# Optimization experiments

Hardware: AMD Instinct MI355X
Metric: run time of the kernel (lower is better)

Reference implementation:

```python
import jax, jax.numpy as jnp
import numpy as np

B, L_HIST, N_VARS, L_FUT = 32, 96, 862, 96
D_MODEL, D_INNER, D_STATE, D_CONV, DT_RANK, D_FF, E_LAYERS = 512, 512, 32, 2, 32, 512, 2
EPS = 1e-5


def _ln(x, w, b):
    m = x.mean(-1, keepdims=True)
    v = ((x - m) ** 2).mean(-1, keepdims=True)
    return (x - m) * jax.lax.rsqrt(v + EPS) * w + b


def _mamba(x, in_w, conv_w, conv_b, x_w, dt_w, dt_b, A_log, D, out_w):
    # x: [B, T, d_model]; standard mamba-ssm selective-scan block (inference)
    Bb, T, _ = x.shape
    u, z = jnp.split(x @ in_w, 2, axis=-1)                      # [B,T,E] each
    uc = jnp.transpose(u, (0, 2, 1))                            # [B,E,T]
    uc = jax.lax.conv_general_dilated(
        uc, conv_w[:, None, :], (1,), [(D_CONV - 1, 0)],
        dimension_numbers=('NCH', 'OIH', 'NCH'),
        feature_group_count=D_INNER)                            # causal depthwise conv
    u = jax.nn.silu(jnp.transpose(uc, (0, 2, 1)) + conv_b)      # [B,T,E]
    dt, Bm, Cm = jnp.split(u @ x_w, [DT_RANK, DT_RANK + D_STATE], axis=-1)
    delta = jax.nn.softplus(dt @ dt_w + dt_b)                   # [B,T,E]
    A = -jnp.exp(A_log)                                         # [E,S]

    def step(h, inp):
        d_t, u_t, B_t, C_t = inp                                # [B,E],[B,E],[B,S],[B,S]
        h = jnp.exp(d_t[..., None] * A) * h + (d_t * u_t)[..., None] * B_t[:, None, :]
        return h, jnp.einsum('bes,bs->be', h, C_t)

    h0 = jnp.zeros((Bb, D_INNER, D_STATE), x.dtype)
    _, ys = jax.lax.scan(step, h0, (delta.transpose(1, 0, 2), u.transpose(1, 0, 2),
                                    Bm.transpose(1, 0, 2), Cm.transpose(1, 0, 2)))
    y = ys.transpose(1, 0, 2) + u * D
    return (y * jax.nn.silu(z)) @ out_w


def _forward(history_data, emb_w, emb_b, m_in_w, m_conv_w, m_conv_b, m_x_w,
             m_dt_w, m_dt_b, m_A_log, m_D, m_out_w, ffn_w1, ffn_b1, ffn_w2,
             ffn_b2, norm1_w, norm1_b, norm2_w, norm2_b, normf_w, normf_b,
             proj_w, proj_b):
    x_enc = history_data[..., 0]                                # [B,L,N]
    means = jax.lax.stop_gradient(x_enc.mean(1, keepdims=True))
    x_enc = x_enc - means
    stdev = jnp.sqrt(x_enc.var(axis=1, keepdims=True) + EPS)
    x_enc = x_enc / stdev
    x = jnp.transpose(x_enc, (0, 2, 1)) @ emb_w + emb_b         # [B,N,d_model] (inverted embed)
    for l in range(E_LAYERS):
        fwd = _mamba(x, m_in_w[l, 0], m_conv_w[l, 0], m_conv_b[l, 0], m_x_w[l, 0],
                     m_dt_w[l, 0], m_dt_b[l, 0], m_A_log[l, 0], m_D[l, 0], m_out_w[l, 0])
        rev = _mamba(x[:, ::-1], m_in_w[l, 1], m_conv_w[l, 1], m_conv_b[l, 1], m_x_w[l, 1],
                     m_dt_w[l, 1], m_dt_b[l, 1], m_A_log[l, 1], m_D[l, 1], m_out_w[l, 1])[:, ::-1]
        x = _ln(x + fwd + rev, norm1_w[l], norm1_b[l])
        y = jax.nn.relu(x @ ffn_w1[l] + ffn_b1[l]) @ ffn_w2[l] + ffn_b2[l]
        x = _ln(x + y, norm2_w[l], norm2_b[l])
    x = _ln(x, normf_w, normf_b)
    dec = jnp.transpose(x @ proj_w + proj_b, (0, 2, 1))         # [B,L_FUT,N]
    dec = dec * stdev[:, 0][:, None, :] + means[:, 0][:, None, :]
    return dec[..., None]                                       # [B,L_FUT,N,1]


def setup_inputs() -> dict:
    key = jax.random.key(0)
    ks = jax.random.split(key, 16)
    def rn(k, shape, s=0.02):
        return jax.random.normal(k, shape, jnp.float32) * s
    M = (E_LAYERS, 2)
    inp = {}
    inp['history_data'] = jax.random.normal(ks[0], (B, L_HIST, N_VARS, 1), jnp.float32)
    inp['emb_w'] = rn(ks[1], (L_HIST, D_MODEL))
    inp['emb_b'] = jnp.zeros((D_MODEL,), jnp.float32)
    inp['m_in_w'] = rn(ks[2], M + (D_MODEL, 2 * D_INNER))
    inp['m_conv_w'] = rn(ks[3], M + (D_INNER, D_CONV), 0.1)
    inp['m_conv_b'] = jnp.zeros(M + (D_INNER,), jnp.float32)
    inp['m_x_w'] = rn(ks[4], M + (D_INNER, DT_RANK + 2 * D_STATE))
    inp['m_dt_w'] = rn(ks[5], M + (DT_RANK, D_INNER), 0.1)
    inp['m_dt_b'] = jnp.full(M + (D_INNER,), -4.0, jnp.float32)
    a = jnp.log(jnp.arange(1, D_STATE + 1, dtype=jnp.float32))
    inp['m_A_log'] = jnp.broadcast_to(a, M + (D_INNER, D_STATE))
    inp['m_D'] = jnp.ones(M + (D_INNER,), jnp.float32)
    inp['m_out_w'] = rn(ks[6], M + (D_INNER, D_MODEL))
    inp['ffn_w1'] = rn(ks[7], (E_LAYERS, D_MODEL, D_FF))
    inp['ffn_b1'] = jnp.zeros((E_LAYERS, D_FF), jnp.float32)
    inp['ffn_w2'] = rn(ks[8], (E_LAYERS, D_FF, D_MODEL))
    inp['ffn_b2'] = jnp.zeros((E_LAYERS, D_MODEL), jnp.float32)
    inp['norm1_w'] = jnp.ones((E_LAYERS, D_MODEL), jnp.float32)
    inp['norm1_b'] = jnp.zeros((E_LAYERS, D_MODEL), jnp.float32)
    inp['norm2_w'] = jnp.ones((E_LAYERS, D_MODEL), jnp.float32)
    inp['norm2_b'] = jnp.zeros((E_LAYERS, D_MODEL), jnp.float32)
    inp['normf_w'] = jnp.ones((D_MODEL,), jnp.float32)
    inp['normf_b'] = jnp.zeros((D_MODEL,), jnp.float32)
    inp['proj_w'] = rn(ks[9], (D_MODEL, L_FUT))
    inp['proj_b'] = jnp.zeros((L_FUT,), jnp.float32)
    return inp


def reference(history_data, emb_w, emb_b, m_in_w, m_conv_w, m_conv_b, m_x_w,
              m_dt_w, m_dt_b, m_A_log, m_D, m_out_w, ffn_w1, ffn_b1, ffn_w2,
              ffn_b2, norm1_w, norm1_b, norm2_w, norm2_b, normf_w, normf_b,
              proj_w, proj_b):
    return _forward(history_data, emb_w, emb_b, m_in_w, m_conv_w, m_conv_b, m_x_w,
                    m_dt_w, m_dt_b, m_A_log, m_D, m_out_w, ffn_w1, ffn_b1, ffn_w2,
                    ffn_b2, norm1_w, norm1_b, norm2_w, norm2_b, normf_w, normf_b,
                    proj_w, proj_b)
```

## Files before the change

kernel.cpp:

```cpp
#include <hip/hip_runtime.h>
#include <math.h>

#define BATCH 32
#define LHIST 96
#define NVARS 862
#define LFUT  96
#define DMODEL 512
#define DINNER 512
#define DSTATE 32
#define DTRANK 32
#define SCAN_C 16
#define SCAN_TC ((NVARS + SCAN_C - 1) / SCAN_C)

typedef short short8 __attribute__((ext_vector_type(8)));
typedef float floatx4 __attribute__((ext_vector_type(4)));
typedef unsigned short ushort;

#define LOG2E 1.44269504088896f

static __device__ __forceinline__ ushort f2b(float f) {
    unsigned u = __builtin_bit_cast(unsigned, f);
    unsigned r = (u + 0x7FFFu + ((u >> 16) & 1u)) >> 16;
    return (ushort)r;
}
static __device__ __forceinline__ float b2f(ushort h) {
    unsigned u = ((unsigned)h) << 16;
    return __builtin_bit_cast(float, u);
}

__global__ void meanstd_k(const float* __restrict__ hist, ushort* __restrict__ xinb,
                          float* __restrict__ meanb, float* __restrict__ stdb,
                          int b0, int CB) {
    int idx = blockIdx.x * blockDim.x + threadIdx.x;
    if (idx >= CB * NVARS) return;
    int b = b0 + idx / NVARS, n = idx % NVARS;
    const float* p = hist + (size_t)b * LHIST * NVARS + n;
    float s = 0.f;
    for (int l = 0; l < LHIST; l++) s += p[(size_t)l * NVARS];
    float mean = s * (1.f / LHIST);
    float v = 0.f;
    for (int l = 0; l < LHIST; l++) { float d = p[(size_t)l * NVARS] - mean; v += d * d; }
    v *= (1.f / LHIST);
    float sd = sqrtf(v + 1e-5f);
    float inv = 1.f / sd;
    meanb[idx] = mean;
    stdb[idx]  = sd;
    ushort* o = xinb + (size_t)idx * LHIST;
    for (int l = 0; l < LHIST; l++) o[l] = f2b((p[(size_t)l * NVARS] - mean) * inv);
}

__global__ void castT_k(const float* __restrict__ W, ushort* __restrict__ Wt,
                        int K, int N, int P) {
    size_t idx = (size_t)blockIdx.x * blockDim.x + threadIdx.x;
    if (idx >= (size_t)P * K * N) return;
    size_t kn = (size_t)K * N;
    int p = (int)(idx / kn);
    int rem = (int)(idx % kn);
    int k = rem / N, n = rem % N;
    Wt[(size_t)p * kn + (size_t)n * K + k] = f2b(W[idx]);
}

__global__ void xw2_cast(const float* __restrict__ xw, ushort* __restrict__ o) {
    int idx = blockIdx.x * blockDim.x + threadIdx.x;
    if (idx >= 2 * 192 * 1024) return;
    int l = idx / (192 * 1024);
    int r = idx % (192 * 1024);
    int n = r / 1024, k = r % 1024;
    int half = (n >= 96);
    int nn = n - 96 * half;
    float v = 0.f;
    if ((k >> 9) == half)
        v = xw[((size_t)(l * 2 + half) * 512 + (k & 511)) * 96 + nn];
    o[idx] = f2b(v);
}

__global__ void dtw2_cast(const float* __restrict__ dtw, ushort* __restrict__ o) {
    int idx = blockIdx.x * blockDim.x + threadIdx.x;
    if (idx >= 2 * 1024 * 192) return;
    int l = idx / (1024 * 192);
    int r = idx % (1024 * 192);
    int n = r / 192, k = r % 192;
    int half = n >> 9;
    int nn = n & 511;
    int kb = k - 96 * half;
    float v = 0.f;
    if (kb >= 0 && kb < 32)
        v = dtw[((size_t)(l * 2 + half) * 32 + kb) * 512 + nn];
    o[idx] = f2b(v);
}

__global__ void outw2_cast(const float* __restrict__ ow, ushort* __restrict__ o) {
    int idx = blockIdx.x * blockDim.x + threadIdx.x;
    if (idx >= 2 * 512 * 1024) return;
    int l = idx / (512 * 1024);
    int r = idx % (512 * 1024);
    int n = r / 1024, k = r % 1024;
    int half = k >> 9;
    float v = ow[((size_t)(l * 2 + half) * 512 + (k & 511)) * 512 + n];
    o[idx] = f2b(v);
}

#define TBM 128
#define TBN 128
#define TBK 32

__global__ __launch_bounds__(256)
void bgemm_k(const ushort* __restrict__ A, int lda,
             const ushort* __restrict__ Bt, int ldb,
             const float* __restrict__ bias,
             float* __restrict__ C, int ldc,
             ushort* __restrict__ C2, int ldc2,
             int M, int N, int K, int act, int accum) {
    __shared__ ushort As[TBM][TBK];
    __shared__ ushort Bs[TBN][TBK];
    int tid = threadIdx.x;
    int gm0 = blockIdx.y * TBM, gn0 = blockIdx.x * TBN;
    int lane = tid & 63, w = tid >> 6;
    int wm = (w >> 1) * 64, wn = (w & 1) * 64;
    int col16 = lane & 15, quad = lane >> 4;

    floatx4 acc[4][4];
#pragma unroll
    for (int i = 0; i < 4; i++)
#pragma unroll
        for (int j = 0; j < 4; j++) acc[i][j] = (floatx4){0.f, 0.f, 0.f, 0.f};

    int srow = tid >> 2;
    int schunk = (tid & 3) * 8;

    for (int k0 = 0; k0 < K; k0 += TBK) {
        int ra0 = min(gm0 + srow, M - 1);
        int ra1 = min(gm0 + srow + 64, M - 1);
        short8 a0 = *(const short8*)(A + (size_t)ra0 * lda + k0 + schunk);
        short8 a1 = *(const short8*)(A + (size_t)ra1 * lda + k0 + schunk);
        int rb0 = min(gn0 + srow, N - 1);
        int rb1 = min(gn0 + srow + 64, N - 1);
        short8 b0 = *(const short8*)(Bt + (size_t)rb0 * ldb + k0 + schunk);
        short8 b1 = *(const short8*)(Bt + (size_t)rb1 * ldb + k0 + schunk);
        __syncthreads();
        *(short8*)&As[srow][schunk]      = a0;
        *(short8*)&As[srow + 64][schunk] = a1;
        *(short8*)&Bs[srow][schunk]      = b0;
        *(short8*)&Bs[srow + 64][schunk] = b1;
        __syncthreads();

        short8 af[4], bf[4];
#pragma unroll
        for (int mt = 0; mt < 4; mt++)
            af[mt] = *(const short8*)&As[wm + mt * 16 + col16][quad * 8];
#pragma unroll
        for (int nt = 0; nt < 4; nt++)
            bf[nt] = *(const short8*)&Bs[wn + nt * 16 + col16][quad * 8];
#pragma unroll
        for (int mt = 0; mt < 4; mt++)
#pragma unroll
            for (int nt = 0; nt < 4; nt++)
                acc[mt][nt] = __builtin_amdgcn_mfma_f32_16x16x32_bf16(
                    af[mt], bf[nt], acc[mt][nt], 0, 0, 0);
    }

    int rbase = gm0 + wm + quad * 4;
    int cbase = gn0 + wn + col16;
#pragma unroll
    for (int mt = 0; mt < 4; mt++) {
#pragma unroll
        for (int reg = 0; reg < 4; reg++) {
            int r = rbase + mt * 16 + reg;
            if (r >= M) continue;
#pragma unroll
            for (int nt = 0; nt < 4; nt++) {
                int c = cbase + nt * 16;
                if (c >= N) continue;
                float v = acc[mt][nt][reg];
                if (bias) v += bias[c];
                if (act == 1) v = fmaxf(v, 0.f);
                else if (act == 2) v = (v > 20.f) ? v : log1pf(expf(v));
                if (accum) v += C[(size_t)r * ldc + c];
                if (C)  C[(size_t)r * ldc + c] = v;
                if (C2) C2[(size_t)r * ldc2 + c] = f2b(v);
            }
        }
    }
}

__global__ void conv8_k(const ushort* __restrict__ uzb2, const float* __restrict__ cw2,
                        const float* __restrict__ cb2, ushort* __restrict__ ucb2, int R) {
    int idx = blockIdx.x * blockDim.x + threadIdx.x;
    if (idx >= R * 128) return;
    int m = idx >> 7;
    int c8 = (idx & 127) * 8;
    int half = c8 >> 9;
    int e0 = c8 & 511;
    int t = m % NVARS;
    const ushort* up = uzb2 + (size_t)m * 2048 + half * 1024 + e0;
    short8 cur = *(const short8*)up;
    short8 oth = (short8){0,0,0,0,0,0,0,0};
    if (!half) { if (t > 0)          oth = *(const short8*)(up - 2048); }
    else       { if (t < NVARS - 1)  oth = *(const short8*)(up + 2048); }
    const float* cw = cw2 + half * 1024;
    const float* cb = cb2 + half * 512;
    short8 res;
#pragma unroll
    for (int i = 0; i < 8; i++) {
        int e = e0 + i;
        float v = cw[e * 2] * b2f((ushort)oth[i]) + cw[e * 2 + 1] * b2f((ushort)cur[i]) + cb[e];
        float sig = 1.f / (1.f + __expf(-v));
        res[i] = (short)f2b(v * sig);
    }
    *(short8*)(ucb2 + (size_t)m * 1024 + c8) = res;
}


static __device__ __forceinline__ bool a_is_fast(const float* A_log2, int col) {
    bool f = true;
#pragma unroll
    for (int s = 0; s < DSTATE; s++) {
        float a = -__expf(A_log2[col * DSTATE + s]);
        f = f && (fabsf(a + (float)(s + 1)) < 1e-3f * (s + 1));
    }
    return f;
}

__global__ __launch_bounds__(256, 4)
void scan_part_k(const ushort* __restrict__ deltab2, const ushort* __restrict__ ucb2,
                 const float* __restrict__ xdbc2, const float* __restrict__ alog2,
                 float* __restrict__ Hpart, float* __restrict__ Sd, int CB) {
    int NP2 = CB * 1024;
    int idx = blockIdx.x * blockDim.x + threadIdx.x;
    if (idx >= NP2 * SCAN_C) return;
    int c = idx / NP2, be = idx % NP2;
    int b = be >> 10, col = be & 1023;
    int rv = col >> 9;

    float h[DSTATE];
#pragma unroll
    for (int s = 0; s < DSTATE; s++) h[s] = 0.f;
    float sd = 0.f;
    int tau1 = min((c + 1) * SCAN_TC, NVARS);
    if (a_is_fast(alog2, col)) {
        for (int tau = c * SCAN_TC; tau < tau1; tau++) {
            int t = rv ? (NVARS - 1 - tau) : tau;
            size_t m = (size_t)b * NVARS + t;
            float d  = b2f(deltab2[m * 1024 + col]);
            float uv = b2f(ucb2[m * 1024 + col]);
            float du = d * uv;
            sd += d;
            const float4* Bp4 = (const float4*)(xdbc2 + m * 192 + rv * 96 + DTRANK);
            float q = __expf(-d), pw = q;
#pragma unroll
            for (int g = 0; g < 8; g++) {
                float4 bv = Bp4[g];
                h[4*g+0] = pw * h[4*g+0] + du * bv.x; pw *= q;
                h[4*g+1] = pw * h[4*g+1] + du * bv.y; pw *= q;
                h[4*g+2] = pw * h[4*g+2] + du * bv.z; pw *= q;
                h[4*g+3] = pw * h[4*g+3] + du * bv.w; if (g < 7) pw *= q;
            }
        }
    } else {
        for (int tau = c * SCAN_TC; tau < tau1; tau++) {
            int t = rv ? (NVARS - 1 - tau) : tau;
            size_t m = (size_t)b * NVARS + t;
            float d  = b2f(deltab2[m * 1024 + col]);
            float uv = b2f(ucb2[m * 1024 + col]);
            float du = d * uv;
            sd += d;
            const float* Bp = xdbc2 + m * 192 + rv * 96 + DTRANK;
#pragma unroll
            for (int s = 0; s < DSTATE; s++) {
                float a2 = -__expf(alog2[col * DSTATE + s]) * LOG2E;
                h[s] = exp2f(d * a2) * h[s] + du * Bp[s];
            }
        }
    }
    Sd[(size_t)c * NP2 + be] = sd;
#pragma unroll
    for (int s = 0; s < DSTATE; s++)
        Hpart[((size_t)c * DSTATE + s) * NP2 + be] = h[s];
}

__global__ __launch_bounds__(256)
void scan_carry_k(float* __restrict__ Hpart, const float* __restrict__ Sd,
                  const float* __restrict__ alog2, int CB) {
    int NP2 = CB * 1024;
    int idx = blockIdx.x * blockDim.x + threadIdx.x;
    if (idx >= NP2 * DSTATE) return;
    int s = idx / NP2, be = idx % NP2;
    int col = be & 1023;
    float a2 = -__expf(alog2[col * DSTATE + s]) * LOG2E;
    float carry = 0.f;
    for (int c = 0; c < SCAN_C; c++) {
        float sd = Sd[(size_t)c * NP2 + be];
        size_t off = ((size_t)c * DSTATE + s) * NP2 + be;
        float hp = Hpart[off];
        Hpart[off] = carry;
        carry = hp + exp2f(a2 * sd) * carry;
    }
}

__global__ __launch_bounds__(256, 4)
void scan_final_k(const ushort* __restrict__ deltab2, const ushort* __restrict__ uzb2,
                  const ushort* __restrict__ ucb2, const float* __restrict__ xdbc2,
                  const float* __restrict__ alog2, const float* __restrict__ Dp2,
                  const float* __restrict__ CarryIn, ushort* __restrict__ yb, int CB) {
    int NP2 = CB * 1024;
    int idx = blockIdx.x * blockDim.x + threadIdx.x;
    if (idx >= NP2 * SCAN_C) return;
    int c = idx / NP2, be = idx % NP2;
    int b = be >> 10, col = be & 1023;
    int rv = col >> 9;

    float h[DSTATE];
#pragma unroll
    for (int s = 0; s < DSTATE; s++)
        h[s] = CarryIn[((size_t)c * DSTATE + s) * NP2 + be];
    float Dv = Dp2[col];
    int tau1 = min((c + 1) * SCAN_TC, NVARS);
    if (a_is_fast(alog2, col)) {
        for (int tau = c * SCAN_TC; tau < tau1; tau++) {
            int t = rv ? (NVARS - 1 - tau) : tau;
            size_t m = (size_t)b * NVARS + t;
            float d  = b2f(deltab2[m * 1024 + col]);
            float zz = b2f(uzb2[m * 2048 + rv * 1024 + 512 + (col & 511)]);
            float uv = b2f(ucb2[m * 1024 + col]);
            float du = d * uv;
            const float4* Bp4 = (const float4*)(xdbc2 + m * 192 + rv * 96 + DTRANK);
            const float4* Cp4 = Bp4 + 8;
            float q = __expf(-d), pw = q;
            float accv = 0.f;
#pragma unroll
            for (int g = 0; g < 8; g++) {
                float4 bv = Bp4[g];
                float4 cv = Cp4[g];
                h[4*g+0] = pw * h[4*g+0] + du * bv.x; accv += h[4*g+0] * cv.x; pw *= q;
                h[4*g+1] = pw * h[4*g+1] + du * bv.y; accv += h[4*g+1] * cv.y; pw *= q;
                h[4*g+2] = pw * h[4*g+2] + du * bv.z; accv += h[4*g+2] * cv.z; pw *= q;
                h[4*g+3] = pw * h[4*g+3] + du * bv.w; accv += h[4*g+3] * cv.w;
                if (g < 7) pw *= q;
            }
            float sig = 1.f / (1.f + __expf(-zz));
            yb[m * 1024 + col] = f2b((accv + uv * Dv) * (zz * sig));
        }
    } else {
        for (int tau = c * SCAN_TC; tau < tau1; tau++) {
            int t = rv ? (NVARS - 1 - tau) : tau;
            size_t m = (size_t)b * NVARS + t;
            float d  = b2f(deltab2[m * 1024 + col]);
            float zz = b2f(uzb2[m * 2048 + rv * 1024 + 512 + (col & 511)]);
            float uv = b2f(ucb2[m * 1024 + col]);
            float du = d * uv;
            const float* Bp = xdbc2 + m * 192 + rv * 96 + DTRANK;
            const float* Cp = Bp + DSTATE;
            float accv = 0.f;
#pragma unroll
            for (int s = 0; s < DSTATE; s++) {
                float a2 = -__expf(alog2[col * DSTATE + s]) * LOG2E;
                h[s] = exp2f(d * a2) * h[s] + du * Bp[s];
                accv += h[s] * Cp[s];
            }
            float sig = 1.f / (1.f + __expf(-zz));
            yb[m * 1024 + col] = f2b((accv + uv * Dv) * (zz * sig));
        }
    }
}

__global__ __launch_bounds__(64)
void ln_k(const float* __restrict__ in1, const float* __restrict__ in2,
          const float* __restrict__ w, const float* __restrict__ b,
          float* __restrict__ out, ushort* __restrict__ outb) {
    int row = blockIdx.x;
    int lane = threadIdx.x;
    const float* p1 = in1 + (size_t)row * DMODEL;
    const float* p2 = in2 ? in2 + (size_t)row * DMODEL : nullptr;
    float v[8];
#pragma unroll
    for (int i = 0; i < 8; i++) {
        int c = lane + i * 64;
        v[i] = p1[c];
        if (p2) v[i] += p2[c];
    }
    float s = 0.f;
#pragma unroll
    for (int i = 0; i < 8; i++) s += v[i];
#pragma unroll
    for (int off = 32; off >= 1; off >>= 1) s += __shfl_xor(s, off);
    float mean = s * (1.f / DMODEL);
    float q = 0.f;
#pragma unroll
    for (int i = 0; i < 8; i++) { float d = v[i] - mean; q += d * d; }
#pragma unroll
    for (int off = 32; off >= 1; off >>= 1) q += __shfl_xor(q, off);
    float rs = rsqrtf(q * (1.f / DMODEL) + 1e-5f);
#pragma unroll
    for (int i = 0; i < 8; i++) {
        int c = lane + i * 64;
        float o = (v[i] - mean) * rs * w[c] + b[c];
        if (out)  out[(size_t)row * DMODEL + c] = o;
        if (outb) outb[(size_t)row * DMODEL + c] = f2b(o);
    }
}

__global__ void final_k(const float* __restrict__ dec, const float* __restrict__ meanb,
                        const float* __restrict__ stdb, float* __restrict__ out,
                        int b0, int CB) {
    int idx = blockIdx.x * blockDim.x + threadIdx.x;
    if (idx >= CB * LFUT * NVARS) return;
    int n = idx % NVARS;
    int r = idx / NVARS;
    int l = r % LFUT;
    int bl = r / LFUT;
    int tok = bl * NVARS + n;
    out[(size_t)((b0 + bl) * LFUT + l) * NVARS + n] =
        dec[(size_t)tok * LFUT + l] * stdb[tok] + meanb[tok];
}

extern "C" void kernel_launch(void* const* d_in, const int* in_sizes, int n_in,
                              void* d_out, int out_size, void* d_ws, size_t ws_size,
                              hipStream_t stream) {
    const float* hist    = (const float*)d_in[0];
    const float* emb_w   = (const float*)d_in[1];
    const float* emb_b   = (const float*)d_in[2];
    const float* m_in_w  = (const float*)d_in[3];
    const float* m_conv_w= (const float*)d_in[4];
    const float* m_conv_b= (const float*)d_in[5];
    const float* m_x_w   = (const float*)d_in[6];
    const float* m_dt_w  = (const float*)d_in[7];
    const float* m_dt_b  = (const float*)d_in[8];
    const float* m_A_log = (const float*)d_in[9];
    const float* m_D     = (const float*)d_in[10];
    const float* m_out_w = (const float*)d_in[11];
    const float* ffn_w1  = (const float*)d_in[12];
    const float* ffn_b1  = (const float*)d_in[13];
    const float* ffn_w2  = (const float*)d_in[14];
    const float* ffn_b2  = (const float*)d_in[15];
    const float* norm1_w = (const float*)d_in[16];
    const float* norm1_b = (const float*)d_in[17];
    const float* norm2_w = (const float*)d_in[18];
    const float* norm2_b = (const float*)d_in[19];
    const float* normf_w = (const float*)d_in[20];
    const float* normf_b = (const float*)d_in[21];
    const float* proj_w  = (const float*)d_in[22];
    const float* proj_b  = (const float*)d_in[23];

    float* out = (float*)d_out;
    float* ws  = (float*)d_ws;

    const size_t WTSE = 4u*1024*512
                      + 2u*512*1024
                      + 2u*512*512 + 2u*512*512
                      + 512u*96
                      + 2u*192*1024
                      + 2u*1024*192
                      + 512u*96;

    int CB = BATCH;
    for (;;) {
        size_t R = (size_t)CB * NVARS, NP2 = (size_t)CB * 1024;
        size_t Rp = (R + 3) & ~3ull;
        size_t fl = R * 1216 + 2 * Rp + (size_t)SCAN_C * 33 * NP2;
        size_t us = R * 4896 + WTSE;
        if (fl * 4 + us * 2 + 1024 <= ws_size || CB == 1) break;
        CB >>= 1;
    }
    const int R   = CB * NVARS;
    const int NP2 = CB * 1024;
    const size_t Rp = ((size_t)R + 3) & ~3ull;

    float* x     = ws;
    float* accb  = x + (size_t)R * 512;
    float* xdbc2 = accb + (size_t)R * 512;
    float* meanb = xdbc2 + (size_t)R * 192;
    float* stdb  = meanb + Rp;
    float* Hpart = stdb + Rp;
    float* Sd    = Hpart + (size_t)SCAN_C * DSTATE * NP2;
    ushort* xb      = (ushort*)(Sd + (size_t)SCAN_C * NP2);
    ushort* uzb2    = xb + (size_t)R * 512;
    ushort* ucb2    = uzb2 + (size_t)R * 2048;
    ushort* deltab2 = ucb2 + (size_t)R * 1024;
    ushort* xinb    = deltab2 + (size_t)R * 1024;
    ushort* xdbc2b  = xinb + (size_t)R * 96;
    ushort* wts     = xdbc2b + (size_t)R * 192;

    ushort *inw_t, *outw2_t, *f1_t, *f2_t, *emb_t, *xw2_t, *dtw2_t, *proj_t;
    {
        ushort* p = wts;
        inw_t   = p; p += (size_t)4 * 1024 * 512;
        outw2_t = p; p += (size_t)2 * 512 * 1024;
        f1_t    = p; p += (size_t)2 * 512 * 512;
        f2_t    = p; p += (size_t)2 * 512 * 512;
        emb_t   = p; p += (size_t)512 * 96;
        xw2_t   = p; p += (size_t)2 * 192 * 1024;
        dtw2_t  = p; p += (size_t)2 * 1024 * 192;
        proj_t  = p;
    }

    castT_k<<<(4 * 512 * 1024 + 255) / 256, 256, 0, stream>>>(m_in_w, inw_t, 512, 1024, 4);
    outw2_cast<<<(2 * 512 * 1024 + 255) / 256, 256, 0, stream>>>(m_out_w, outw2_t);
    castT_k<<<(2 * 512 * 512 + 255) / 256, 256, 0, stream>>>(ffn_w1, f1_t, 512, 512, 2);
    castT_k<<<(2 * 512 * 512 + 255) / 256, 256, 0, stream>>>(ffn_w2, f2_t, 512, 512, 2);
    castT_k<<<(96 * 512 + 255) / 256, 256, 0, stream>>>(emb_w, emb_t, 96, 512, 1);
    xw2_cast<<<(2 * 192 * 1024 + 255) / 256, 256, 0, stream>>>(m_x_w, xw2_t);
    dtw2_cast<<<(2 * 1024 * 192 + 255) / 256, 256, 0, stream>>>(m_dt_w, dtw2_t);
    castT_k<<<(512 * 96 + 255) / 256, 256, 0, stream>>>(proj_w, proj_t, 512, 96, 1);

    auto bgemm = [&](const ushort* A, int lda, const ushort* Bt, int ldb,
                     const float* bias, float* C, int ldc, ushort* C2, int ldc2,
                     int M, int N, int K, int act, int accum) {
        dim3 grid((N + TBN - 1) / TBN, (M + TBM - 1) / TBM);
        bgemm_k<<<grid, 256, 0, stream>>>(A, lda, Bt, ldb, bias, C, ldc, C2, ldc2,
                                          M, N, K, act, accum);
    };

    for (int b0 = 0; b0 < BATCH; b0 += CB) {
        meanstd_k<<<(R + 255) / 256, 256, 0, stream>>>(hist, xinb, meanb, stdb, b0, CB);
        bgemm(xinb, 96, emb_t, 96, emb_b, x, 512, xb, 512, R, 512, 96, 0, 0);

        for (int l = 0; l < 2; l++) {
            const float* cw2   = m_conv_w + (size_t)l * 2048;
            const float* cb2   = m_conv_b + (size_t)l * 1024;
            const float* dtb2  = m_dt_b  + (size_t)l * 1024;
            const float* alog2 = m_A_log + (size_t)l * 2 * 512 * 32;
            const float* Dp2   = m_D     + (size_t)l * 1024;

            bgemm(xb, 512, inw_t + (size_t)(2 * l) * 1024 * 512, 512, nullptr,
                  nullptr, 0, uzb2, 2048, R, 2048, 512, 0, 0);
            conv8_k<<<(R * 128 + 255) / 256, 256, 0, stream>>>(uzb2, cw2, cb2, ucb2, R);
            bgemm(ucb2, 1024, xw2_t + (size_t)l * 192 * 1024, 1024, nullptr,
                  xdbc2, 192, xdbc2b, 192, R, 192, 1024, 0, 0);
            bgemm(xdbc2b, 192, dtw2_t + (size_t)l * 1024 * 192, 192, dtb2,
                  nullptr, 0, deltab2, 1024, R, 1024, 192, 2, 0);
            scan_part_k<<<(NP2 * SCAN_C + 255) / 256, 256, 0, stream>>>(
                deltab2, ucb2, xdbc2, alog2, Hpart, Sd, CB);
            scan_carry_k<<<(NP2 * DSTATE + 255) / 256, 256, 0, stream>>>(
                Hpart, Sd, alog2, CB);
            scan_final_k<<<(NP2 * SCAN_C + 255) / 256, 256, 0, stream>>>(
                deltab2, uzb2, ucb2, xdbc2, alog2, Dp2, Hpart, deltab2, CB);
            bgemm(deltab2, 1024, outw2_t + (size_t)l * 512 * 1024, 1024, nullptr,
                  accb, 512, nullptr, 0, R, 512, 1024, 0, 0);

            ln_k<<<R, 64, 0, stream>>>(accb, x, norm1_w + l * DMODEL, norm1_b + l * DMODEL,
                                       x, xb);
            bgemm(xb, 512, f1_t + (size_t)l * 512 * 512, 512, ffn_b1 + l * DMODEL,
                  nullptr, 0, ucb2, 512, R, 512, 512, 1, 0);
            bgemm(ucb2, 512, f2_t + (size_t)l * 512 * 512, 512, ffn_b2 + l * DMODEL,
                  accb, 512, nullptr, 0, R, 512, 512, 0, 0);
            ln_k<<<R, 64, 0, stream>>>(x, accb, norm2_w + l * DMODEL, norm2_b + l * DMODEL,
                                       x, xb);
        }

        ln_k<<<R, 64, 0, stream>>>(x, nullptr, normf_w, normf_b, nullptr, xb);
        bgemm(xb, 512, proj_t, 512, proj_b, xdbc2, 96, nullptr, 0, R, 96, 512, 0, 0);
        final_k<<<(CB * LFUT * NVARS + 255) / 256, 256, 0, stream>>>(
            xdbc2, meanb, stdb, out, b0, CB);
    }
}
```

Before: 2.531 ms.

## Double-buffer shared memory tiles in bf16 GEMM with register prefetch

```diff
diff --git a/kernel.cpp b/kernel.cpp
--- a/kernel.cpp
+++ b/kernel.cpp
@@ -111,8 +111,8 @@
              float* __restrict__ C, int ldc,
              ushort* __restrict__ C2, int ldc2,
              int M, int N, int K, int act, int accum) {
-    __shared__ ushort As[TBM][TBK];
-    __shared__ ushort Bs[TBN][TBK];
+    __shared__ ushort As[2][TBM][TBK];
+    __shared__ ushort Bs[2][TBN][TBK];
     int tid = threadIdx.x;
     int gm0 = blockIdx.y * TBM, gn0 = blockIdx.x * TBN;
     int lane = tid & 63, w = tid >> 6;
@@ -128,29 +128,55 @@
     int srow = tid >> 2;
     int schunk = (tid & 3) * 8;
 
-    for (int k0 = 0; k0 < K; k0 += TBK) {
-        int ra0 = min(gm0 + srow, M - 1);
-        int ra1 = min(gm0 + srow + 64, M - 1);
-        short8 a0 = *(const short8*)(A + (size_t)ra0 * lda + k0 + schunk);
-        short8 a1 = *(const short8*)(A + (size_t)ra1 * lda + k0 + schunk);
-        int rb0 = min(gn0 + srow, N - 1);
-        int rb1 = min(gn0 + srow + 64, N - 1);
-        short8 b0 = *(const short8*)(Bt + (size_t)rb0 * ldb + k0 + schunk);
-        short8 b1 = *(const short8*)(Bt + (size_t)rb1 * ldb + k0 + schunk);
+    const ushort* pa0 = A + (size_t)min(gm0 + srow, M - 1) * lda + schunk;
+    const ushort* pa1 = A + (size_t)min(gm0 + srow + 64, M - 1) * lda + schunk;
+    const ushort* pb0 = Bt + (size_t)min(gn0 + srow, N - 1) * ldb + schunk;
+    const ushort* pb1 = Bt + (size_t)min(gn0 + srow + 64, N - 1) * ldb + schunk;
+
+    int nk = K / TBK;
+
+    short8 ra0 = *(const short8*)pa0;
+    short8 ra1 = *(const short8*)pa1;
+    short8 rb0 = *(const short8*)pb0;
+    short8 rb1 = *(const short8*)pb1;
+    *(short8*)&As[0][srow][schunk]      = ra0;
+    *(short8*)&As[0][srow + 64][schunk] = ra1;
+    *(short8*)&Bs[0][srow][schunk]      = rb0;
+    *(short8*)&Bs[0][srow + 64][schunk] = rb1;
+    if (nk > 1) {
+        ra0 = *(const short8*)(pa0 + TBK);
+        ra1 = *(const short8*)(pa1 + TBK);
+        rb0 = *(const short8*)(pb0 + TBK);
+        rb1 = *(const short8*)(pb1 + TBK);
+    }
+
+    for (int it = 0; it < nk; it++) {
         __syncthreads();
-        *(short8*)&As[srow][schunk]      = a0;
-        *(short8*)&As[srow + 64][schunk] = a1;
-        *(short8*)&Bs[srow][schunk]      = b0;
-        *(short8*)&Bs[srow + 64][schunk] = b1;
-        __syncthreads();
+        int cur = it & 1;
 
         short8 af[4], bf[4];
 #pragma unroll
         for (int mt = 0; mt < 4; mt++)
-            af[mt] = *(const short8*)&As[wm + mt * 16 + col16][quad * 8];
+            af[mt] = *(const short8*)&As[cur][wm + mt * 16 + col16][quad * 8];
 #pragma unroll
         for (int nt = 0; nt < 4; nt++)
-            bf[nt] = *(const short8*)&Bs[wn + nt * 16 + col16][quad * 8];
+            bf[nt] = *(const short8*)&Bs[cur][wn + nt * 16 + col16][quad * 8];
+
+        if (it + 1 < nk) {
+            int nxt = cur ^ 1;
+            *(short8*)&As[nxt][srow][schunk]      = ra0;
+            *(short8*)&As[nxt][srow + 64][schunk] = ra1;
+            *(short8*)&Bs[nxt][srow][schunk]      = rb0;
+            *(short8*)&Bs[nxt][srow + 64][schunk] = rb1;
+        }
+        if (it + 2 < nk) {
+            int k2 = (it + 2) * TBK;
+            ra0 = *(const short8*)(pa0 + k2);
+            ra1 = *(const short8*)(pa1 + k2);
+            rb0 = *(const short8*)(pb0 + k2);
+            rb1 = *(const short8*)(pb1 + k2);
+        }
+
 #pragma unroll
         for (int mt = 0; mt < 4; mt++)
 #pragma unroll
```

Measured after the change: 2.401 ms. 1.05x faster.
